# Kernel optimization log

Measured on AMD Instinct MI355X. Metric: run time of the kernel, lower is better.

The kernel has to match this reference:

```python
import jax, jax.numpy as jnp
import numpy as np

WS = 7           # window_size
NUM_HEADS = 4
DIM = 128
BNW = 4096       # batch * num_windows
NW = 64          # windows per image (attn_mask leading dim)
N = WS * WS      # tokens per window = 49


def make_rel_idx(ws: int) -> np.ndarray:
    coords = np.stack(np.meshgrid(np.arange(ws), np.arange(ws), indexing='ij'))  # (2, ws, ws)
    flat = coords.reshape(2, -1)                                                  # (2, N)
    rel = flat[:, :, None] - flat[:, None, :]                                     # (2, N, N)
    rel = rel.transpose(1, 2, 0).copy()
    rel[:, :, 0] += ws - 1
    rel[:, :, 1] += ws - 1
    rel[:, :, 0] *= 2 * ws - 1
    return rel.sum(-1).astype(np.int32)                                           # (N, N)


def setup_inputs() -> dict:
    key = jax.random.key(0)
    ks = jax.random.split(key, 4)
    x = jax.random.normal(ks[0], (BNW, N, DIM), dtype=jnp.float32)
    attn_mask = jnp.zeros((NW, N, N), dtype=jnp.float32)
    qkv_w = jax.random.normal(ks[1], (3 * DIM, DIM), dtype=jnp.float32) * 0.02
    qkv_b = jnp.zeros((3 * DIM,), dtype=jnp.float32)
    proj_w = jax.random.normal(ks[2], (DIM, DIM), dtype=jnp.float32) * 0.02
    proj_b = jnp.zeros((DIM,), dtype=jnp.float32)
    bias_table = jax.random.normal(ks[3], ((2 * WS - 1) ** 2, NUM_HEADS), dtype=jnp.float32) * 0.02
    rel_idx = jnp.asarray(make_rel_idx(WS))
    return {"x": x, "attn_mask": attn_mask, "qkv_w": qkv_w, "qkv_b": qkv_b,
            "proj_w": proj_w, "proj_b": proj_b, "bias_table": bias_table,
            "rel_idx": rel_idx}


def reference(x, attn_mask, qkv_w, qkv_b, proj_w, proj_b, bias_table, rel_idx):
    BnW, n, C = x.shape
    H = NUM_HEADS
    hd = C // H
    scale = hd ** -0.5
    # qkv projection: (BnW, n, 3C) -> (3, BnW, H, n, hd)
    qkv = (x @ qkv_w.T + qkv_b).reshape(BnW, n, 3, H, hd).transpose(2, 0, 3, 1, 4)
    q, k, v = qkv[0], qkv[1], qkv[2]
    attn = jnp.einsum('bhnd,bhmd->bhnm', q * scale, k)          # (BnW, H, n, n)
    bias = bias_table[rel_idx]                                   # (n, n, H)
    attn = attn + bias.transpose(2, 0, 1)[None]                  # broadcast (1, H, n, n)
    nW = attn_mask.shape[0]
    attn = attn.reshape(-1, nW, H, n, n) + attn_mask[None, :, None]
    attn = attn.reshape(-1, H, n, n)
    attn = jax.nn.softmax(attn, axis=-1)
    out = jnp.einsum('bhnm,bhmd->bhnd', attn, v)                 # (BnW, H, n, hd)
    out = out.transpose(0, 2, 1, 3).reshape(BnW, n, C)
    return out @ proj_w.T + proj_b
```

## Files before the change

kernel.cpp:

```cpp
#include <hip/hip_runtime.h>

#define NT   49
#define HD   32
#define NH   4
#define DIM  128
#define SCALEQ 0.17677669529663687f

typedef __attribute__((ext_vector_type(8))) short short8;
typedef __attribute__((ext_vector_type(4))) short short4v;
typedef __attribute__((ext_vector_type(4))) float floatx4;
typedef short8 short8a __attribute__((may_alias));
typedef short4v short4a __attribute__((may_alias));
typedef unsigned long long ulla __attribute__((may_alias));
typedef unsigned long long ull;

__device__ __forceinline__ short f2b(float f) {
    union { float f; unsigned u; } v; v.f = f;
    return (short)((v.u + 0x7fffu + ((v.u >> 16) & 1u)) >> 16);
}
__device__ __forceinline__ float b2f(short s) {
    union { unsigned u; float f; } v; v.u = ((unsigned)(unsigned short)s) << 16;
    return v.f;
}

__global__ __launch_bounds__(256) void wmsa_prep(
        const float* __restrict__ qkvw, const float* __restrict__ projw,
        const float* __restrict__ btab, const int* __restrict__ ridx,
        const float* __restrict__ mask,
        short* __restrict__ wqkv, short* __restrict__ wproj,
        short* __restrict__ cmb) {
    __shared__ __align__(16) int   s_ridx[NT * NT];
    __shared__ __align__(16) float s_btab[169 * 4];
    __shared__ __align__(16) float s_mask[NT * NT];

    const int wdw = blockIdx.x;
    const int tid = threadIdx.x;

    {
        int g = wdw * 256 + tid;
        const float* src = (g < 12288) ? (qkvw + g * 4) : (projw + (g - 12288) * 4);
        float4 v = *(const float4*)src;
        float s = (g < 4096) ? SCALEQ : 1.0f;
        ull pk =  (ull)(unsigned short)f2b(v.x * s)
                | ((ull)(unsigned short)f2b(v.y * s) << 16)
                | ((ull)(unsigned short)f2b(v.z * s) << 32)
                | ((ull)(unsigned short)f2b(v.w * s) << 48);
        if (g < 12288) *(ulla*)(wqkv + g * 4) = pk;
        else           *(ulla*)(wproj + (g - 12288) * 4) = pk;
    }

    for (int i = tid; i < NT * NT; i += 256) s_ridx[i] = ridx[i];
    for (int i = tid; i < 169 * 4; i += 256) s_btab[i] = btab[i];
    {
        const float* mw = mask + (size_t)wdw * NT * NT;
        for (int i = tid; i < NT * NT; i += 256) s_mask[i] = mw[i];
    }
    __syncthreads();

    #pragma unroll
    for (int gi = 0; gi < 4; ++gi) {
        int g = gi * 256 + tid;
        int cc = g & 15, qq = (g >> 4) & 3, tile = g >> 6;
        int it = tile >> 2, jt = tile & 3;
        int col = jt * 16 + cc;
        int rowb = it * 16 + qq * 4;
        if (col >= NT) {
            ull m16 = (unsigned short)f2b(-1e30f);
            ull pk = m16 | (m16 << 16) | (m16 << 32) | (m16 << 48);
            #pragma unroll
            for (int h = 0; h < NH; ++h)
                *(ulla*)(cmb + (((size_t)wdw * NH + h) << 12) + g * 4) = pk;
        } else {
            float bt[4][4], mv[4];
            #pragma unroll
            for (int r = 0; r < 4; ++r) {
                int row = rowb + r;
                if (row >= NT) {
                    bt[r][0] = bt[r][1] = bt[r][2] = bt[r][3] = 0.f;
                    mv[r] = 0.f;
                } else {
                    int ri = s_ridx[row * NT + col];
                    float4 b4 = *(const float4*)(s_btab + ri * 4);
                    bt[r][0] = b4.x; bt[r][1] = b4.y; bt[r][2] = b4.z; bt[r][3] = b4.w;
                    mv[r] = s_mask[row * NT + col];
                }
            }
            #pragma unroll
            for (int h = 0; h < NH; ++h) {
                ull pk =  (ull)(unsigned short)f2b(bt[0][h] + mv[0])
                        | ((ull)(unsigned short)f2b(bt[1][h] + mv[1]) << 16)
                        | ((ull)(unsigned short)f2b(bt[2][h] + mv[2]) << 32)
                        | ((ull)(unsigned short)f2b(bt[3][h] + mv[3]) << 48);
                *(ulla*)(cmb + (((size_t)wdw * NH + h) << 12) + g * 4) = pk;
            }
        }
    }
}

#define RWAVE 12800
#define OSTR  136
#define LDSB  51200

__global__ __launch_bounds__(256, 3) void wmsa_main(
    const float* __restrict__ x,
    const float* __restrict__ qkvb, const float* __restrict__ projb,
    const short* __restrict__ wqkv, const short* __restrict__ wproj,
    const short* __restrict__ cmb, float* __restrict__ out)
{
    __shared__ __align__(16) char pool[LDSB];
    short* lds = (short*)pool;

    const int b    = blockIdx.x;
    const int wdw  = b & 63;
    const int tid  = threadIdx.x;
    const int wave = tid >> 6;
    const int lane = tid & 63;
    const int qq   = lane >> 4;
    const int cc   = lane & 15;
    const int ccl  = cc & 7, cch = cc >> 3, cm3 = cc & 3;

    const int colbase = wave * 32 + cc;
    short8 bfc[4], bfn[4];
    #pragma unroll
    for (int ks = 0; ks < 4; ++ks)
        bfc[ks] = *(const short8a*)(wqkv + colbase * DIM + ks * 32 + qq * 8);
    float biasv[6];
    #pragma unroll
    for (int j = 0; j < 6; ++j)
        biasv[j] = qkvb[(j >> 1) * DIM + colbase + (j & 1) * 16];

    {
        const float* xb = x + (size_t)b * NT * DIM;
        for (int i = tid; i < NT * 32; i += 256) {
            int t = i >> 5, c4 = (i & 31) << 2;
            float4 v = *(const float4*)(xb + t * DIM + c4);
            ull pk =  (ull)(unsigned short)f2b(v.x)
                    | ((ull)(unsigned short)f2b(v.y) << 16)
                    | ((ull)(unsigned short)f2b(v.z) << 32)
                    | ((ull)(unsigned short)f2b(v.w) << 48);
            *(ulla*)(lds + t * 136 + c4) = pk;
        }
        for (int i = tid; i < (64 - NT) * 32; i += 256) {
            int t = NT + (i >> 5), c4 = (i & 31) << 2;
            *(ulla*)(lds + t * 136 + c4) = 0ull;
        }
    }
    __syncthreads();

    short8 af[4][4];
    #pragma unroll
    for (int it = 0; it < 4; ++it)
        #pragma unroll
        for (int ks = 0; ks < 4; ++ks)
            af[it][ks] = *(const short8a*)(lds + (it * 16 + cc) * 136 + ks * 32 + qq * 8);
    __syncthreads();

    short* qw = (short*)(pool + wave * RWAVE);
    short* kw = qw + 2048;
    short* vw = qw + 4096;
    short* pw = qw;

    short4v cm[16];
    {
        const short* cw = cmb + (((size_t)wdw * NH + wave) << 12);
        #pragma unroll
        for (int t16 = 0; t16 < 16; ++t16)
            cm[t16] = *(const short4a*)(cw + t16 * 256 + qq * 64 + cc * 4);
    }

    #pragma unroll
    for (int jt6 = 0; jt6 < 6; ++jt6) {
        const int sec = jt6 >> 1, hlf = jt6 & 1;
        if (jt6 < 5) {
            const int cn = ((jt6 + 1) >> 1) * DIM + colbase + ((jt6 + 1) & 1) * 16;
            #pragma unroll
            for (int ks = 0; ks < 4; ++ks)
                bfn[ks] = *(const short8a*)(wqkv + cn * DIM + ks * 32 + qq * 8);
        }
        float bias = biasv[jt6];
        if (sec == 0) bias *= SCALEQ;
        const floatx4 cinit = {bias, bias, bias, bias};
        #pragma unroll
        for (int it = 0; it < 4; ++it) {
            floatx4 acc = cinit;
            #pragma unroll
            for (int ks = 0; ks < 4; ++ks)
                acc = __builtin_amdgcn_mfma_f32_16x16x32_bf16(af[it][ks], bfc[ks], acc, 0, 0, 0);
            if (sec == 2) {
                int dd = hlf * 16 + cc;
                int t0 = it * 16 + qq * 4;
                ull pk =  (ull)(unsigned short)f2b(acc[0])
                        | ((ull)(unsigned short)f2b(acc[1]) << 16)
                        | ((ull)(unsigned short)f2b(acc[2]) << 32)
                        | ((ull)(unsigned short)f2b(acc[3]) << 48);
                *(ulla*)(vw + dd * 72 + t0) = pk;
            } else {
                short* dst = (sec == 0) ? qw : kw;
                int gb = hlf * 2 + cch;
                #pragma unroll
                for (int r = 0; r < 4; ++r) {
                    int t = it * 16 + qq * 4 + r;
                    dst[t * 32 + ((gb ^ r) << 3) + ccl] = f2b(acc[r]);
                }
            }
        }
        #pragma unroll
        for (int ks = 0; ks < 4; ++ks) bfc[ks] = bfn[ks];
    }

    __asm__ volatile("" ::: "memory");

    {
        short8 qf[4], kf[4];
        #pragma unroll
        for (int t = 0; t < 4; ++t) {
            qf[t] = *(const short8a*)(qw + (t * 16 + cc) * 32 + ((qq ^ cm3) << 3));
            kf[t] = *(const short8a*)(kw + (t * 16 + cc) * 32 + ((qq ^ cm3) << 3));
        }
        #pragma unroll
        for (int it = 0; it < 4; ++it) {
            floatx4 s[4];
            #pragma unroll
            for (int jt = 0; jt < 4; ++jt) {
                short4v cb = cm[it * 4 + jt];
                floatx4 ci = {b2f(cb.x), b2f(cb.y), b2f(cb.z), b2f(cb.w)};
                s[jt] = __builtin_amdgcn_mfma_f32_16x16x32_bf16(qf[it], kf[jt], ci, 0, 0, 0);
            }
            #pragma unroll
            for (int r = 0; r < 4; ++r) {
                int t = it * 16 + qq * 4 + r;
                #pragma unroll
                for (int jt = 0; jt < 4; ++jt) {
                    float ee = __expf(s[jt][r]);
                    int g = (jt * 2 + cch) ^ r;
                    pw[t * 64 + (g << 3) + ccl] = f2b(ee);
                }
            }
        }
    }
    __asm__ volatile("" ::: "memory");

    floatx4 o[4][2], ssum[4];
    #pragma unroll
    for (int it = 0; it < 4; ++it) {
        o[it][0] = (floatx4){0.f, 0.f, 0.f, 0.f};
        o[it][1] = (floatx4){0.f, 0.f, 0.f, 0.f};
        ssum[it] = (floatx4){0.f, 0.f, 0.f, 0.f};
    }
    const short BONE = (short)0x3F80;
    const short8 onesf = {BONE, BONE, BONE, BONE, BONE, BONE, BONE, BONE};
    #pragma unroll
    for (int ks = 0; ks < 2; ++ks) {
        short8 pf[4], vf[2];
        #pragma unroll
        for (int it = 0; it < 4; ++it)
            pf[it] = *(const short8a*)(pw + (it * 16 + cc) * 64 + (((ks * 4 + qq) ^ cm3) << 3));
        #pragma unroll
        for (int jv = 0; jv < 2; ++jv)
            vf[jv] = *(const short8a*)(vw + (jv * 16 + cc) * 72 + ks * 32 + qq * 8);
        #pragma unroll
        for (int it = 0; it < 4; ++it) {
            o[it][0] = __builtin_amdgcn_mfma_f32_16x16x32_bf16(pf[it], vf[0], o[it][0], 0, 0, 0);
            o[it][1] = __builtin_amdgcn_mfma_f32_16x16x32_bf16(pf[it], vf[1], o[it][1], 0, 0, 0);
            ssum[it] = __builtin_amdgcn_mfma_f32_16x16x32_bf16(pf[it], onesf, ssum[it], 0, 0, 0);
        }
    }
    #pragma unroll
    for (int it = 0; it < 4; ++it)
        #pragma unroll
        for (int r = 0; r < 4; ++r) {
            float inv = 1.0f / ssum[it][r];
            o[it][0][r] *= inv;
            o[it][1][r] *= inv;
        }

    short8 pcur[4], pnxt[4];
    float pbv[8];
    #pragma unroll
    for (int ks = 0; ks < 4; ++ks) {
        pcur[ks] = *(const short8a*)(wproj + cc * DIM + ks * 32 + qq * 8);
        pnxt[ks] = *(const short8a*)(wproj + (16 + cc) * DIM + ks * 32 + qq * 8);
    }
    #pragma unroll
    for (int j = 0; j < 8; ++j) pbv[j] = projb[j * 16 + cc];

    __syncthreads();

    short* ow = (short*)pool;
    #pragma unroll
    for (int it = 0; it < 4; ++it)
        #pragma unroll
        for (int jv = 0; jv < 2; ++jv)
            #pragma unroll
            for (int r = 0; r < 4; ++r) {
                int t = it * 16 + qq * 4 + r;
                ow[t * OSTR + wave * 32 + jv * 16 + cc] = f2b(o[it][jv][r]);
            }
    __syncthreads();

    {
        short8 a2[4];
        #pragma unroll
        for (int ks = 0; ks < 4; ++ks)
            a2[ks] = *(const short8a*)(ow + (wave * 16 + cc) * OSTR + ks * 32 + qq * 8);
        float* outb = out + (size_t)b * NT * DIM;
        #pragma unroll
        for (int jt = 0; jt < 8; ++jt) {
            short8 pfut[4];
            if (jt < 6) {
                int cn = (jt + 2) * 16 + cc;
                #pragma unroll
                for (int ks = 0; ks < 4; ++ks)
                    pfut[ks] = *(const short8a*)(wproj + cn * DIM + ks * 32 + qq * 8);
            }
            float pb = pbv[jt];
            floatx4 acc = {pb, pb, pb, pb};
            #pragma unroll
            for (int ks = 0; ks < 4; ++ks)
                acc = __builtin_amdgcn_mfma_f32_16x16x32_bf16(a2[ks], pcur[ks], acc, 0, 0, 0);
            int col = jt * 16 + cc;
            #pragma unroll
            for (int r = 0; r < 4; ++r) {
                int row = wave * 16 + qq * 4 + r;
                if (row < NT) outb[row * DIM + col] = acc[r];
            }
            #pragma unroll
            for (int ks = 0; ks < 4; ++ks) { pcur[ks] = pnxt[ks]; pnxt[ks] = pfut[ks]; }
        }
    }
}

extern "C" void kernel_launch(void* const* d_in, const int* in_sizes, int n_in,
                              void* d_out, int out_size, void* d_ws, size_t ws_size,
                              hipStream_t stream) {
    const float* x     = (const float*)d_in[0];
    const float* mask  = (const float*)d_in[1];
    const float* qkvw  = (const float*)d_in[2];
    const float* qkvb  = (const float*)d_in[3];
    const float* projw = (const float*)d_in[4];
    const float* projb = (const float*)d_in[5];
    const float* btab  = (const float*)d_in[6];
    const int*   ridx  = (const int*)d_in[7];
    float* outp = (float*)d_out;

    short* wqkv  = (short*)d_ws;
    short* wproj = (short*)((char*)d_ws + 98304);
    short* cmb   = (short*)((char*)d_ws + 131072);

    wmsa_prep<<<64, 256, 0, stream>>>(qkvw, projw, btab, ridx, mask, wqkv, wproj, cmb);
    wmsa_main<<<4096, 256, 0, stream>>>(x, qkvb, projb, wqkv, wproj, cmb, outp);
}
```

Before: 300.2 us.

## Keep V in registers via 16x16x16 MFMA, shrink LDS to raise occupancy

V is no longer staged in LDS. The QKV projection accumulator fragments are kept in registers and fed directly as B operands to 16x16x16 bf16 MFMAs for the P·V product. The P swizzle is adjusted so the new 4-element reads stay conflict-free. Per-wave LDS shrinks from 12800 to 8192 bytes, which allows launch bounds of 5 blocks per CU instead of 3. The trade-off is twice as many half-size MFMA instructions, more live registers (vq, plus cm loaded later) and possible spills under the tighter register budget.

```diff
diff --git a/kernel.cpp b/kernel.cpp
--- a/kernel.cpp
+++ b/kernel.cpp
@@ -22,6 +22,18 @@
     union { unsigned u; float f; } v; v.u = ((unsigned)(unsigned short)s) << 16;
     return v.f;
 }
+
+#if __has_builtin(__builtin_amdgcn_mfma_f32_16x16x16bf16_1k)
+__device__ __forceinline__ floatx4 MFMA16(short4v a, short4v b, floatx4 c) {
+    return __builtin_amdgcn_mfma_f32_16x16x16bf16_1k(a, b, c, 0, 0, 0);
+}
+#else
+__device__ __forceinline__ floatx4 MFMA16(short4v a, short4v b, floatx4 c) {
+    short8 a8 = {a[0], a[1], a[2], a[3], 0, 0, 0, 0};
+    short8 b8 = {b[0], b[1], b[2], b[3], 0, 0, 0, 0};
+    return __builtin_amdgcn_mfma_f32_16x16x32_bf16(a8, b8, c, 0, 0, 0);
+}
+#endif
 
 __global__ __launch_bounds__(256) void wmsa_prep(
         const float* __restrict__ qkvw, const float* __restrict__ projw,
@@ -97,11 +109,11 @@
     }
 }
 
-#define RWAVE 12800
+#define RWAVE 8192
 #define OSTR  136
-#define LDSB  51200
-
-__global__ __launch_bounds__(256, 3) void wmsa_main(
+#define LDSB  32768
+
+__global__ __launch_bounds__(256, 5) void wmsa_main(
     const float* __restrict__ x,
     const float* __restrict__ qkvb, const float* __restrict__ projb,
     const short* __restrict__ wqkv, const short* __restrict__ wproj,
@@ -157,16 +169,9 @@
 
     short* qw = (short*)(pool + wave * RWAVE);
     short* kw = qw + 2048;
-    short* vw = qw + 4096;
     short* pw = qw;
 
-    short4v cm[16];
-    {
-        const short* cw = cmb + (((size_t)wdw * NH + wave) << 12);
-        #pragma unroll
-        for (int t16 = 0; t16 < 16; ++t16)
-            cm[t16] = *(const short4a*)(cw + t16 * 256 + qq * 64 + cc * 4);
-    }
+    short4v vq[2][4];
 
     #pragma unroll
     for (int jt6 = 0; jt6 < 6; ++jt6) {
@@ -187,13 +192,10 @@
             for (int ks = 0; ks < 4; ++ks)
                 acc = __builtin_amdgcn_mfma_f32_16x16x32_bf16(af[it][ks], bfc[ks], acc, 0, 0, 0);
             if (sec == 2) {
-                int dd = hlf * 16 + cc;
-                int t0 = it * 16 + qq * 4;
-                ull pk =  (ull)(unsigned short)f2b(acc[0])
-                        | ((ull)(unsigned short)f2b(acc[1]) << 16)
-                        | ((ull)(unsigned short)f2b(acc[2]) << 32)
-                        | ((ull)(unsigned short)f2b(acc[3]) << 48);
-                *(ulla*)(vw + dd * 72 + t0) = pk;
+                short4v pv;
+                pv[0] = f2b(acc[0]); pv[1] = f2b(acc[1]);
+                pv[2] = f2b(acc[2]); pv[3] = f2b(acc[3]);
+                vq[hlf][it] = pv;
             } else {
                 short* dst = (sec == 0) ? qw : kw;
                 int gb = hlf * 2 + cch;
@@ -208,6 +210,13 @@
         for (int ks = 0; ks < 4; ++ks) bfc[ks] = bfn[ks];
     }
 
+    short4v cm[16];
+    {
+        const short* cw = cmb + (((size_t)wdw * NH + wave) << 12);
+        #pragma unroll
+        for (int t16 = 0; t16 < 16; ++t16)
+            cm[t16] = *(const short4a*)(cw + t16 * 256 + qq * 64 + cc * 4);
+    }
     __asm__ volatile("" ::: "memory");
 
     {
@@ -232,7 +241,7 @@
                 #pragma unroll
                 for (int jt = 0; jt < 4; ++jt) {
                     float ee = __expf(s[jt][r]);
-                    int g = (jt * 2 + cch) ^ r;
+                    int g = (jt * 2 + cch) ^ r ^ ((qq & 1) << 2);
                     pw[t * 64 + (g << 3) + ccl] = f2b(ee);
                 }
             }
@@ -248,21 +257,16 @@
         ssum[it] = (floatx4){0.f, 0.f, 0.f, 0.f};
     }
     const short BONE = (short)0x3F80;
-    const short8 onesf = {BONE, BONE, BONE, BONE, BONE, BONE, BONE, BONE};
-    #pragma unroll
-    for (int ks = 0; ks < 2; ++ks) {
-        short8 pf[4], vf[2];
-        #pragma unroll
-        for (int it = 0; it < 4; ++it)
-            pf[it] = *(const short8a*)(pw + (it * 16 + cc) * 64 + (((ks * 4 + qq) ^ cm3) << 3));
-        #pragma unroll
-        for (int jv = 0; jv < 2; ++jv)
-            vf[jv] = *(const short8a*)(vw + (jv * 16 + cc) * 72 + ks * 32 + qq * 8);
-        #pragma unroll
-        for (int it = 0; it < 4; ++it) {
-            o[it][0] = __builtin_amdgcn_mfma_f32_16x16x32_bf16(pf[it], vf[0], o[it][0], 0, 0, 0);
-            o[it][1] = __builtin_amdgcn_mfma_f32_16x16x32_bf16(pf[it], vf[1], o[it][1], 0, 0, 0);
-            ssum[it] = __builtin_amdgcn_mfma_f32_16x16x32_bf16(pf[it], onesf, ssum[it], 0, 0, 0);
+    const short4v ones4 = {BONE, BONE, BONE, BONE};
+    #pragma unroll
+    for (int rt = 0; rt < 4; ++rt) {
+        #pragma unroll
+        for (int kt = 0; kt < 4; ++kt) {
+            int g = (kt * 2 + (qq >> 1)) ^ cm3 ^ (((cc >> 2) & 1) << 2);
+            short4v pf = *(const short4a*)(pw + (rt * 16 + cc) * 64 + (g << 3) + (qq & 1) * 4);
+            o[rt][0] = MFMA16(pf, vq[0][kt], o[rt][0]);
+            o[rt][1] = MFMA16(pf, vq[1][kt], o[rt][1]);
+            ssum[rt] = MFMA16(pf, ones4, ssum[rt]);
         }
     }
     #pragma unroll
```

Result: slower. 529.1 us (+76.2%).
